# Performance work log

Measured on AMD Instinct MI355X. Metric: run time of the kernel, lower is better.

## Reference

```python
import jax, jax.numpy as jnp
import numpy as np

T, I, H, O = 16384, 2048, 2048, 1000


def setup_inputs() -> dict:
    key = jax.random.key(0)
    ks = jax.random.split(key, 4)
    lim_r = 1.0 / np.sqrt(H)  # equinox GRUCell uniform init bound
    lim_l = 1.0 / np.sqrt(H)
    return {
        "x": jax.random.normal(ks[0], (T, I), dtype=jnp.float32),
        "weight_ih": jax.random.uniform(ks[1], (3 * H, I), minval=-lim_r, maxval=lim_r, dtype=jnp.float32),
        "weight_hh": jax.random.uniform(ks[2], (3 * H, H), minval=-lim_r, maxval=lim_r, dtype=jnp.float32),
        "bias": jnp.zeros((3 * H,), jnp.float32),
        "bias_n": jnp.zeros((H,), jnp.float32),
        "w_out": jax.random.uniform(ks[3], (O, H), minval=-lim_l, maxval=lim_l, dtype=jnp.float32),
        "b_out": jnp.zeros((O,), jnp.float32),
        "bias_extra": jnp.zeros((O,), jnp.float32),
    }


def reference(x, weight_ih, weight_hh, bias, bias_n, w_out, b_out, bias_extra):
    h_dim = weight_hh.shape[1]
    # input-side gate pre-activations for all timesteps at once: (T, 3H)
    igates = x @ weight_ih.T + bias

    def step(h, ig):
        hg = weight_hh @ h  # (3H,)
        ir, iz, inn = jnp.split(ig, 3)
        hr, hz, hn = jnp.split(hg, 3)
        r = jax.nn.sigmoid(ir + hr)
        z = jax.nn.sigmoid(iz + hz)
        n = jnp.tanh(inn + r * (hn + bias_n))
        return n + z * (h - n), None  # equinox GRUCell update

    h0 = jnp.zeros((h_dim,), x.dtype)
    h_final, _ = jax.lax.scan(step, h0, igates)
    return w_out @ h_final + b_out + bias_extra
```

## Files before the change

### kernel.cpp

```cpp
#include <hip/hip_runtime.h>
#include <hip/hip_bf16.h>

typedef unsigned int u32;
typedef unsigned short u16;
typedef unsigned long long u64;
using half2_t = __attribute__((ext_vector_type(2))) _Float16;
using half8   = __attribute__((ext_vector_type(8))) _Float16;
using f32x4   = __attribute__((ext_vector_type(4))) float;
using u32x4   = __attribute__((ext_vector_type(4))) u32;

#define TT 16384
#define HDIM 2048
#define N3H 6144
#define ODIM 1000

#define WS_WPACK 0ull
#define WS_PROG  25165824ull
#define WS_IG    117440512ull
#define WS_PAIR  318767104ull
#define WS_NEED  318785536ull

#if __has_builtin(__builtin_amdgcn_fdot2)
__device__ __forceinline__ float fdot2u(u32 a, u32 b, float c) {
  return __builtin_amdgcn_fdot2(__builtin_bit_cast(half2_t, a),
                                __builtin_bit_cast(half2_t, b), c, false);
}
#else
__device__ __forceinline__ float fdot2u(u32 a, u32 b, float c) {
  half2_t x = __builtin_bit_cast(half2_t, a), y = __builtin_bit_cast(half2_t, b);
  return c + (float)x[0] * (float)y[0] + (float)x[1] * (float)y[1];
}
#endif

__device__ __forceinline__ u32x4 poll_load16(const u32* p) {
  u32x4 r;
  asm volatile("global_load_dwordx4 %0, %1, off sc0 sc1\n\ts_waitcnt vmcnt(0)"
               : "=&v"(r) : "v"(p));
  return r;
}
__device__ __forceinline__ u32 cload4_cp(const u32* p) {
  u32 r;
  asm volatile("global_load_dword %0, %1, off sc0 sc1\n\ts_waitcnt vmcnt(0)"
               : "=&v"(r) : "v"(p));
  return r;
}
__device__ __forceinline__ void ld3_f16_cp(const _Float16* p0, const _Float16* p1,
                                           const _Float16* p2, float& a, float& b, float& c) {
  u32 ra, rb, rc;
  asm volatile("global_load_ushort %0, %3, off sc0 sc1\n\t"
               "global_load_ushort %1, %4, off sc0 sc1\n\t"
               "global_load_ushort %2, %5, off sc0 sc1\n\t"
               "s_waitcnt vmcnt(0)"
               : "=&v"(ra), "=&v"(rb), "=&v"(rc)
               : "v"(p0), "v"(p1), "v"(p2));
  a = (float)__builtin_bit_cast(_Float16, (u16)ra);
  b = (float)__builtin_bit_cast(_Float16, (u16)rb);
  c = (float)__builtin_bit_cast(_Float16, (u16)rc);
}
__device__ __forceinline__ void st2_cp(_Float16* p, _Float16 v) {
  u32 u = (u32)__builtin_bit_cast(u16, v);
  asm volatile("global_store_short %0, %1, off sc0 sc1" :: "v"(p), "v"(u) : "memory");
}

__global__ void k_zero(u32* p) {
  p[blockIdx.x * 256 + threadIdx.x] = 0u;
}
__global__ void k_zero_n(u32* p, int n) {
  int i = blockIdx.x * 256 + threadIdx.x;
  if (i < n) p[i] = 0u;
}

__global__ __launch_bounds__(256) void k_pack(const float* __restrict__ whh,
                                              u32* __restrict__ outp) {
  u32 idx = blockIdx.x * 256 + threadIdx.x;
  u32 hrow = idx / 3072;
  u32 rem = idx - hrow * 3072;
  u32 c = rem >> 8;
  u32 lane = (rem >> 2) & 63;
  u32 q = rem & 3;
  u32 dl = c * 4 + q;
  u32 g = dl >> 4;
  u32 m = dl & 15;
  u32 kp = lane * 16 + m;
  const float* src = whh + (size_t)(g * 2048 + hrow) * 2048 + 2 * kp;
  half2_t p;
  p[0] = (_Float16)src[0];
  p[1] = (_Float16)src[1];
  outp[idx] = __builtin_bit_cast(u32, p);
}

__device__ __forceinline__ u32 packf16(float a, float b) {
  half2_t p;
  p[0] = (_Float16)a;
  p[1] = (_Float16)b;
  return __builtin_bit_cast(u32, p);
}

__global__ __launch_bounds__(512) void k_fused(const uint4* __restrict__ wpack,
                                               const _Float16* __restrict__ ig,
                                               const float* __restrict__ bias_n,
                                               u32* pair,
                                               const float* __restrict__ X,
                                               const float* __restrict__ Wih,
                                               const float* __restrict__ bias,
                                               u32* prog) {
  __shared__ __align__(16) u32 smem[4096];
  const int tid = threadIdx.x;

  if (blockIdx.x < 128) {
    u32* lds_h = smem;
    const int l = tid & 63, v = tid >> 6;
    const int wg = blockIdx.x;
    const int r0 = wg * 16 + v * 2;
    const int my_row = r0 + (l & 1);

    u32 wdwA[48], wdwB[48];
    {
      const uint4* wpA = wpack + (size_t)r0 * 768 + l;
      const uint4* wpB = wpA + 768;
#pragma unroll
      for (int c = 0; c < 12; ++c) {
        uint4 a = wpA[(size_t)c * 64];
        wdwA[c * 4] = a.x; wdwA[c * 4 + 1] = a.y; wdwA[c * 4 + 2] = a.z; wdwA[c * 4 + 3] = a.w;
      }
#pragma unroll
      for (int c = 0; c < 12; ++c) {
        uint4 b = wpB[(size_t)c * 64];
        wdwB[c * 4] = b.x; wdwB[c * 4 + 1] = b.y; wdwB[c * 4 + 2] = b.z; wdwB[c * 4 + 3] = b.w;
      }
    }
    const float bn = bias_n[my_row];
    float hm = 0.f;
    u32 hreg[16];
#pragma unroll
    for (int m = 0; m < 16; ++m) hreg[m] = 0;

    int ready_blk = 0;
    {
      for (;;) {
        u32 c = cload4_cp(prog);
        if (c >= 48u) break;
        __builtin_amdgcn_s_sleep(8);
      }
      ready_blk = 1;
    }
    float ig0, ig1, ig2;
    ld3_f16_cp(ig + my_row, ig + 2048 + my_row, ig + 4096 + my_row, ig0, ig1, ig2);

    for (int t = 0; t < TT; ++t) {
      float igr = ig0, igz = ig1, ign = ig2;
      float a0 = 0.f, a1 = 0.f, a2 = 0.f, a3 = 0.f, a4 = 0.f, a5 = 0.f;
      float b0 = 0.f, b1 = 0.f, b2 = 0.f, b3 = 0.f, b4 = 0.f, b5 = 0.f;
#pragma unroll
      for (int m = 0; m < 16; m += 2) {
        a0 = fdot2u(wdwA[m],          hreg[m],     a0);
        b0 = fdot2u(wdwA[m + 1],      hreg[m + 1], b0);
        a1 = fdot2u(wdwA[16 + m],     hreg[m],     a1);
        b1 = fdot2u(wdwA[16 + m + 1], hreg[m + 1], b1);
        a2 = fdot2u(wdwA[32 + m],     hreg[m],     a2);
        b2 = fdot2u(wdwA[32 + m + 1], hreg[m + 1], b2);
        a3 = fdot2u(wdwB[m],          hreg[m],     a3);
        b3 = fdot2u(wdwB[m + 1],      hreg[m + 1], b3);
        a4 = fdot2u(wdwB[16 + m],     hreg[m],     a4);
        b4 = fdot2u(wdwB[16 + m + 1], hreg[m + 1], b4);
        a5 = fdot2u(wdwB[32 + m],     hreg[m],     a5);
        b5 = fdot2u(wdwB[32 + m + 1], hreg[m + 1], b5);
      }
      float s0 = a0 + b0, s1 = a1 + b1, s2 = a2 + b2;
      float s3 = a3 + b3, s4 = a4 + b4, s5 = a5 + b5;
#pragma unroll
      for (int off = 1; off < 64; off <<= 1) {
        s0 += __shfl_xor(s0, off, 64);
        s1 += __shfl_xor(s1, off, 64);
        s2 += __shfl_xor(s2, off, 64);
        s3 += __shfl_xor(s3, off, 64);
        s4 += __shfl_xor(s4, off, 64);
        s5 += __shfl_xor(s5, off, 64);
      }
      u32* pdst = pair + (((t + 1) & 1) << 11);
      u32 pk = 0;
      if (l < 2) {
        float sr = l ? s3 : s0, sz = l ? s4 : s1, sn = l ? s5 : s2;
        float r = 1.f / (1.f + __expf(-(igr + sr)));
        float z = 1.f / (1.f + __expf(-(igz + sz)));
        float nx = ign + r * (sn + bn);
        float e = __expf(-2.f * nx);
        float n = (1.f - e) / (1.f + e);
        hm = n + z * (hm - n);
        pk = ((u32)(t + 1) << 16) | (u32)__builtin_bit_cast(u16, (_Float16)hm);
      }
      u32 pk1 = __shfl(pk, 1, 64);
      if (l == 0)
        __hip_atomic_store((u64*)(pdst + r0), (u64)pk | ((u64)pk1 << 32),
                           __ATOMIC_RELAXED, __HIP_MEMORY_SCOPE_AGENT);
      if (t == TT - 1) break;
      {
        int nb = (t + 1) >> 7;
        if (nb >= ready_blk) {
          const u32* pb = prog + nb;
          for (;;) {
            u32 c = cload4_cp(pb);
            if (c >= 48u) break;
            __builtin_amdgcn_s_sleep(8);
          }
          ready_blk = nb + 1;
        }
        const _Float16* igp = ig + (size_t)(t + 1) * N3H;
        ld3_f16_cp(igp + my_row, igp + 2048 + my_row, igp + 4096 + my_row, ig0, ig1, ig2);
      }
      const u32 tgt = (u32)(t + 1) << 16;
      const u32* pp = pdst + 4 * tid;
      __builtin_amdgcn_s_sleep(2);
      u32x4 d;
      for (;;) {
        d = poll_load16(pp);
        u32 bad = ((d[0] ^ tgt) | (d[1] ^ tgt) | (d[2] ^ tgt) | (d[3] ^ tgt)) & 0xFFFF0000u;
        if (!bad) break;
        __builtin_amdgcn_s_sleep(2);
      }
      __syncthreads();
      u32 p0 = (d[0] & 0xFFFFu) | (d[1] << 16);
      u32 p1 = (d[2] & 0xFFFFu) | (d[3] << 16);
      u32* dst = lds_h + 2 * tid + ((tid >> 3) << 2);
      dst[0] = p0;
      dst[1] = p1;
      __syncthreads();
#pragma unroll
      for (int i = 0; i < 4; ++i) {
        uint4 vv = *(const uint4*)(lds_h + l * 20 + i * 4);
        hreg[i * 4] = vv.x; hreg[i * 4 + 1] = vv.y; hreg[i * 4 + 2] = vv.z; hreg[i * 4 + 3] = vv.w;
      }
    }
  } else {
    _Float16* As = (_Float16*)smem;
    _Float16* Bs = (_Float16*)(smem + 2048);
    const int hid = blockIdx.x - 128;
    const int l = tid & 63, w = tid >> 6;
    const int wr = w >> 2, wc = w & 3;
    const int srow = tid >> 2;
    const int scol = (tid & 3) << 3;

    for (int tile = hid; tile < 6144; tile += 128) {
      const int mb = tile / 48, nb = tile - mb * 48;
      const int m0 = mb * 128, n0 = nb * 128;
      f32x4 acc[4][2] = {};

      for (int k0 = 0; k0 < HDIM; k0 += 32) {
        __syncthreads();
        const float* ap = X + (size_t)(m0 + srow) * HDIM + k0 + scol;
        const float* bp = Wih + (size_t)(n0 + srow) * HDIM + k0 + scol;
        float4 aL = *(const float4*)ap, aH = *(const float4*)(ap + 4);
        float4 bL = *(const float4*)bp, bH = *(const float4*)(bp + 4);
        uint4 av4 = make_uint4(packf16(aL.x, aL.y), packf16(aL.z, aL.w),
                               packf16(aH.x, aH.y), packf16(aH.z, aH.w));
        uint4 bv4 = make_uint4(packf16(bL.x, bL.y), packf16(bL.z, bL.w),
                               packf16(bH.x, bH.y), packf16(bH.z, bH.w));
        *(uint4*)(As + srow * 32 + scol) = av4;
        *(uint4*)(Bs + srow * 32 + scol) = bv4;
        __syncthreads();
        half8 av[4], bv[2];
#pragma unroll
        for (int mi = 0; mi < 4; ++mi)
          av[mi] = *(const half8*)(As + (wr * 64 + mi * 16 + (l & 15)) * 32 + (l >> 4) * 8);
#pragma unroll
        for (int ni = 0; ni < 2; ++ni)
          bv[ni] = *(const half8*)(Bs + (wc * 32 + ni * 16 + (l & 15)) * 32 + (l >> 4) * 8);
#pragma unroll
        for (int mi = 0; mi < 4; ++mi)
#pragma unroll
          for (int ni = 0; ni < 2; ++ni)
            acc[mi][ni] = __builtin_amdgcn_mfma_f32_16x16x32_f16(av[mi], bv[ni], acc[mi][ni], 0, 0, 0);
      }
      _Float16* Cout = (_Float16*)ig;
#pragma unroll
      for (int ni = 0; ni < 2; ++ni) {
        int col = n0 + wc * 32 + ni * 16 + (l & 15);
        float bb = bias[col];
#pragma unroll
        for (int mi = 0; mi < 4; ++mi) {
          int rbase = m0 + wr * 64 + mi * 16 + (l >> 4) * 4;
#pragma unroll
          for (int r = 0; r < 4; ++r)
            st2_cp(Cout + (size_t)(rbase + r) * N3H + col,
                   (_Float16)(acc[mi][ni][r] + bb));
        }
      }
      asm volatile("s_waitcnt vmcnt(0)" ::: "memory");
      __syncthreads();
      if (tid == 0)
        __hip_atomic_fetch_add(prog + mb, 1u, __ATOMIC_RELAXED,
                               __HIP_MEMORY_SCOPE_AGENT);
    }
  }
}

__global__ __launch_bounds__(256) void k_out(const float* __restrict__ wout,
                                             const float* __restrict__ bout,
                                             const float* __restrict__ bextra,
                                             const u32* __restrict__ hp,
                                             float* __restrict__ out) {
  const int l = threadIdx.x & 63;
  const int o = blockIdx.x * 4 + (threadIdx.x >> 6);
  if (o >= ODIM) return;
  const float* wr = wout + (size_t)o * HDIM;
  float acc = 0.f;
#pragma unroll
  for (int i = 0; i < 8; ++i) {
    int k4 = i * 256 + l * 4;
    uint4 hd = *(const uint4*)(hp + k4);
    float4 wv = *(const float4*)(wr + k4);
    acc += wv.x * (float)__builtin_bit_cast(_Float16, (u16)(hd.x & 0xFFFFu));
    acc += wv.y * (float)__builtin_bit_cast(_Float16, (u16)(hd.y & 0xFFFFu));
    acc += wv.z * (float)__builtin_bit_cast(_Float16, (u16)(hd.z & 0xFFFFu));
    acc += wv.w * (float)__builtin_bit_cast(_Float16, (u16)(hd.w & 0xFFFFu));
  }
#pragma unroll
  for (int off = 1; off < 64; off <<= 1) acc += __shfl_xor(acc, off, 64);
  if (l == 0) out[o] = acc + bout[o] + bextra[o];
}

__global__ void k_dbg(float* out, float v) {
  int i = blockIdx.x * 256 + threadIdx.x;
  if (i < ODIM) out[i] = v;
}

extern "C" void kernel_launch(void* const* d_in, const int* in_sizes, int n_in,
                              void* d_out, int out_size, void* d_ws, size_t ws_size,
                              hipStream_t stream) {
  const float* x      = (const float*)d_in[0];
  const float* wih    = (const float*)d_in[1];
  const float* whh    = (const float*)d_in[2];
  const float* bias   = (const float*)d_in[3];
  const float* bias_n = (const float*)d_in[4];
  const float* wout   = (const float*)d_in[5];
  const float* bout   = (const float*)d_in[6];
  const float* bextra = (const float*)d_in[7];
  float* out = (float*)d_out;

  if (ws_size < WS_NEED) {
    k_dbg<<<4, 256, 0, stream>>>(out, 1.0e6f + (float)(ws_size / 1048576ull));
    return;
  }

  char* ws = (char*)d_ws;
  u32*      wpack = (u32*)(ws + WS_WPACK);
  u32*      prog  = (u32*)(ws + WS_PROG);
  _Float16* igb   = (_Float16*)(ws + WS_IG);
  u32*      pairb = (u32*)(ws + WS_PAIR);

  k_zero<<<16, 256, 0, stream>>>(pairb);
  k_zero_n<<<1, 256, 0, stream>>>(prog, 128);
  k_pack<<<24576, 256, 0, stream>>>(whh, wpack);

  const uint4* wpc = (const uint4*)wpack;
  const _Float16* igc = igb;
  void* kargs[] = {(void*)&wpc, (void*)&igc, (void*)&bias_n, (void*)&pairb,
                   (void*)&x, (void*)&wih, (void*)&bias, (void*)&prog};
  hipLaunchCooperativeKernel(k_fused, dim3(256), dim3(512), kargs, 0, stream);

  k_out<<<250, 256, 0, stream>>>(wout, bout, bextra, pairb, out);
}
```

Before: 42.99 ms.

## Halve recurrent workgroups, give each wave four hidden rows, widen GEMM pool

The persistent GRU recurrence now runs on 64 workgroups instead of 128. Each wave keeps register-resident fp16 weights for four hidden rows instead of two, and publishes its four tagged h values with a single 16-byte store. The blocks freed this way move to the input-projection GEMM (192 instead of 128) so the gate pre-activations are produced faster. The trade is that each timestep's dot-product and reduction work per wave doubles, and register pressure rises to about 192 weight registers per lane, which risks spills or longer critical-path latency in the serial recurrence.

```diff
diff --git a/kernel.cpp b/kernel.cpp
--- a/kernel.cpp
+++ b/kernel.cpp
@@ -60,6 +60,9 @@
 __device__ __forceinline__ void st2_cp(_Float16* p, _Float16 v) {
   u32 u = (u32)__builtin_bit_cast(u16, v);
   asm volatile("global_store_short %0, %1, off sc0 sc1" :: "v"(p), "v"(u) : "memory");
+}
+__device__ __forceinline__ void st16_cp(u32* p, u32x4 v) {
+  asm volatile("global_store_dwordx4 %0, %1, off sc0 sc1" :: "v"(p), "v"(v) : "memory");
 }
 
 __global__ void k_zero(u32* p) {
@@ -107,26 +110,25 @@
   __shared__ __align__(16) u32 smem[4096];
   const int tid = threadIdx.x;
 
-  if (blockIdx.x < 128) {
+  if (blockIdx.x < 64) {
     u32* lds_h = smem;
     const int l = tid & 63, v = tid >> 6;
     const int wg = blockIdx.x;
-    const int r0 = wg * 16 + v * 2;
-    const int my_row = r0 + (l & 1);
-
-    u32 wdwA[48], wdwB[48];
+    const int r0 = wg * 32 + v * 4;
+    const int my_row = r0 + (l & 3);
+
+    u32 wdw[4][48];
     {
-      const uint4* wpA = wpack + (size_t)r0 * 768 + l;
-      const uint4* wpB = wpA + 768;
-#pragma unroll
-      for (int c = 0; c < 12; ++c) {
-        uint4 a = wpA[(size_t)c * 64];
-        wdwA[c * 4] = a.x; wdwA[c * 4 + 1] = a.y; wdwA[c * 4 + 2] = a.z; wdwA[c * 4 + 3] = a.w;
-      }
-#pragma unroll
-      for (int c = 0; c < 12; ++c) {
-        uint4 b = wpB[(size_t)c * 64];
-        wdwB[c * 4] = b.x; wdwB[c * 4 + 1] = b.y; wdwB[c * 4 + 2] = b.z; wdwB[c * 4 + 3] = b.w;
+      const uint4* wp0 = wpack + (size_t)r0 * 768 + l;
+#pragma unroll
+      for (int j = 0; j < 4; ++j) {
+        const uint4* wpj = wp0 + j * 768;
+#pragma unroll
+        for (int c = 0; c < 12; ++c) {
+          uint4 a = wpj[(size_t)c * 64];
+          wdw[j][c * 4] = a.x; wdw[j][c * 4 + 1] = a.y;
+          wdw[j][c * 4 + 2] = a.z; wdw[j][c * 4 + 3] = a.w;
+        }
       }
     }
     const float bn = bias_n[my_row];
@@ -149,38 +151,30 @@
 
     for (int t = 0; t < TT; ++t) {
       float igr = ig0, igz = ig1, ign = ig2;
-      float a0 = 0.f, a1 = 0.f, a2 = 0.f, a3 = 0.f, a4 = 0.f, a5 = 0.f;
-      float b0 = 0.f, b1 = 0.f, b2 = 0.f, b3 = 0.f, b4 = 0.f, b5 = 0.f;
-#pragma unroll
-      for (int m = 0; m < 16; m += 2) {
-        a0 = fdot2u(wdwA[m],          hreg[m],     a0);
-        b0 = fdot2u(wdwA[m + 1],      hreg[m + 1], b0);
-        a1 = fdot2u(wdwA[16 + m],     hreg[m],     a1);
-        b1 = fdot2u(wdwA[16 + m + 1], hreg[m + 1], b1);
-        a2 = fdot2u(wdwA[32 + m],     hreg[m],     a2);
-        b2 = fdot2u(wdwA[32 + m + 1], hreg[m + 1], b2);
-        a3 = fdot2u(wdwB[m],          hreg[m],     a3);
-        b3 = fdot2u(wdwB[m + 1],      hreg[m + 1], b3);
-        a4 = fdot2u(wdwB[16 + m],     hreg[m],     a4);
-        b4 = fdot2u(wdwB[16 + m + 1], hreg[m + 1], b4);
-        a5 = fdot2u(wdwB[32 + m],     hreg[m],     a5);
-        b5 = fdot2u(wdwB[32 + m + 1], hreg[m + 1], b5);
-      }
-      float s0 = a0 + b0, s1 = a1 + b1, s2 = a2 + b2;
-      float s3 = a3 + b3, s4 = a4 + b4, s5 = a5 + b5;
+      float s[12];
+#pragma unroll
+      for (int i = 0; i < 12; ++i) s[i] = 0.f;
+#pragma unroll
+      for (int m = 0; m < 16; ++m) {
+        u32 h = hreg[m];
+#pragma unroll
+        for (int j = 0; j < 4; ++j) {
+          s[3 * j + 0] = fdot2u(wdw[j][m],      h, s[3 * j + 0]);
+          s[3 * j + 1] = fdot2u(wdw[j][16 + m], h, s[3 * j + 1]);
+          s[3 * j + 2] = fdot2u(wdw[j][32 + m], h, s[3 * j + 2]);
+        }
+      }
 #pragma unroll
       for (int off = 1; off < 64; off <<= 1) {
-        s0 += __shfl_xor(s0, off, 64);
-        s1 += __shfl_xor(s1, off, 64);
-        s2 += __shfl_xor(s2, off, 64);
-        s3 += __shfl_xor(s3, off, 64);
-        s4 += __shfl_xor(s4, off, 64);
-        s5 += __shfl_xor(s5, off, 64);
+#pragma unroll
+        for (int i = 0; i < 12; ++i) s[i] += __shfl_xor(s[i], off, 64);
       }
       u32* pdst = pair + (((t + 1) & 1) << 11);
       u32 pk = 0;
-      if (l < 2) {
-        float sr = l ? s3 : s0, sz = l ? s4 : s1, sn = l ? s5 : s2;
+      if (l < 4) {
+        float sr = l == 0 ? s[0] : l == 1 ? s[3] : l == 2 ? s[6] : s[9];
+        float sz = l == 0 ? s[1] : l == 1 ? s[4] : l == 2 ? s[7] : s[10];
+        float sn = l == 0 ? s[2] : l == 1 ? s[5] : l == 2 ? s[8] : s[11];
         float r = 1.f / (1.f + __expf(-(igr + sr)));
         float z = 1.f / (1.f + __expf(-(igz + sz)));
         float nx = ign + r * (sn + bn);
@@ -190,9 +184,13 @@
         pk = ((u32)(t + 1) << 16) | (u32)__builtin_bit_cast(u16, (_Float16)hm);
       }
       u32 pk1 = __shfl(pk, 1, 64);
-      if (l == 0)
-        __hip_atomic_store((u64*)(pdst + r0), (u64)pk | ((u64)pk1 << 32),
-                           __ATOMIC_RELAXED, __HIP_MEMORY_SCOPE_AGENT);
+      u32 pk2 = __shfl(pk, 2, 64);
+      u32 pk3 = __shfl(pk, 3, 64);
+      if (l == 0) {
+        u32x4 pv;
+        pv[0] = pk; pv[1] = pk1; pv[2] = pk2; pv[3] = pk3;
+        st16_cp(pdst + r0, pv);
+      }
       if (t == TT - 1) break;
       {
         int nb = (t + 1) >> 7;
@@ -234,13 +232,13 @@
   } else {
     _Float16* As = (_Float16*)smem;
     _Float16* Bs = (_Float16*)(smem + 2048);
-    const int hid = blockIdx.x - 128;
+    const int hid = blockIdx.x - 64;
     const int l = tid & 63, w = tid >> 6;
     const int wr = w >> 2, wc = w & 3;
     const int srow = tid >> 2;
     const int scol = (tid & 3) << 3;
 
-    for (int tile = hid; tile < 6144; tile += 128) {
+    for (int tile = hid; tile < 6144; tile += 192) {
       const int mb = tile / 48, nb = tile - mb * 48;
       const int m0 = mb * 128, n0 = nb * 128;
       f32x4 acc[4][2] = {};
```

Result: slower. 63.72 ms (+48.2%).
